# Optimization experiments

Hardware: AMD Instinct MI355X
Metric: run time of the kernel (lower is better)

## Reference

```python
import jax, jax.numpy as jnp
import numpy as np

N_NODES = 50000
N_EDGES = 1600000
N_FEAT = 4
N_GRAPHS = 128
K = 5


def setup_inputs() -> dict:
    key = jax.random.key(0)
    ks = jax.random.split(key, 16)
    x = jax.random.normal(ks[0], (N_NODES, N_FEAT), dtype=jnp.float32)
    edge_index = jax.random.randint(ks[1], (2, N_EDGES), 0, N_NODES, dtype=jnp.int64)
    batch = jnp.sort(jax.random.randint(ks[2], (N_NODES,), 0, N_GRAPHS, dtype=jnp.int64))
    def lin(k, shape):
        fan_in = shape[-2]
        return jax.random.normal(k, shape, dtype=jnp.float32) / np.sqrt(fan_in)
    return {
        "x": x,
        "edge_index": edge_index,
        "batch": batch,
        "num_graphs": N_GRAPHS,
        "W1": lin(ks[3], (K, N_FEAT, 32)), "b1": jnp.zeros((32,), jnp.float32),
        "W2": lin(ks[4], (K, 32, 64)),     "b2": jnp.zeros((64,), jnp.float32),
        "W3": lin(ks[5], (K, 64, 64)),     "b3": jnp.zeros((64,), jnp.float32),
        "fcw1": lin(ks[6], (64, 32)), "fcb1": jnp.zeros((32,), jnp.float32),
        "fcw2": lin(ks[7], (32, 1)),  "fcb2": jnp.zeros((1,), jnp.float32),
    }


def _cheb_conv(h, src, dst, w, Wk, b, n_nodes):
    # PyG ChebConv with sym norm, lambda_max=2:
    #   L_hat h = scatter_add(w_e * h[src_e] -> dst_e), w_e = -dinv[src]*dinv[dst]
    def L(z):
        return jax.ops.segment_sum(w[:, None] * z[src], dst, num_segments=n_nodes)
    Tx0 = h
    Tx1 = L(h)
    out = jnp.einsum('nf,fo->no', Tx0, Wk[0]) + jnp.einsum('nf,fo->no', Tx1, Wk[1])
    for k in range(2, Wk.shape[0]):
        Tx2 = 2.0 * L(Tx1) - Tx0
        out = out + jnp.einsum('nf,fo->no', Tx2, Wk[k])
        Tx0, Tx1 = Tx1, Tx2
    return out + b


def reference(x, edge_index, batch, num_graphs, W1, b1, W2, b2, W3, b3,
              fcw1, fcb1, fcw2, fcb2):
    n = x.shape[0]
    src, dst = edge_index[0], edge_index[1]
    # remove self loops (PyG ChebConv does remove_self_loops first)
    ew = (src != dst).astype(x.dtype)
    deg = jax.ops.segment_sum(ew, src, num_segments=n)
    dinv = jnp.where(deg > 0, jax.lax.rsqrt(jnp.where(deg > 0, deg, 1.0)), 0.0)
    w = -ew * dinv[src] * dinv[dst]  # scaled Laplacian off-diagonal; diagonal is 0

    h = jax.nn.relu(_cheb_conv(x, src, dst, w, W1, b1, n))
    h = jax.nn.relu(_cheb_conv(h, src, dst, w, W2, b2, n))
    h = jax.nn.relu(_cheb_conv(h, src, dst, w, W3, b3, n))

    # global_mean_pool over graph segments
    sums = jax.ops.segment_sum(h, batch, num_segments=num_graphs)
    cnts = jax.ops.segment_sum(jnp.ones((n,), h.dtype), batch, num_segments=num_graphs)
    pooled = sums / jnp.maximum(cnts, 1.0)[:, None]

    h = jax.nn.relu(pooled @ fcw1 + fcb1)
    return h @ fcw2 + fcb2
```

## Files before the change

kernel.cpp:

```cpp
#include <hip/hip_runtime.h>


constexpr int N_NODES  = 50000;
constexpr int N_EDGES  = 1600000;
constexpr int N_GRAPHS = 128;

constexpr int N16  = N_NODES * 16;
constexpr int SB32 = (N_NODES + 31) / 32;

constexpr int NB_H = 256;
constexpr int EPB  = N_EDGES / NB_H;
constexpr int NW   = (N_NODES + 3) / 4;

static inline int cdiv(long long a, int b) { return (int)((a + b - 1) / b); }


__global__ __launch_bounds__(256) void hist2_kernel(const int* __restrict__ src,
                                                    const int* __restrict__ dst,
                                                    unsigned* __restrict__ Hs,
                                                    unsigned* __restrict__ Hd) {
    extern __shared__ unsigned lds2[];
    unsigned* ls = lds2;
    unsigned* ld_ = lds2 + NW;
    const int b = blockIdx.x, t = threadIdx.x;
    for (int i = t; i < 2 * NW; i += 256) lds2[i] = 0;
    __syncthreads();
    const int e0 = b * EPB, e1 = e0 + EPB;
    for (int e = e0 + t; e < e1; e += 256) {
        int s = src[e], d = dst[e];
        if (s != d) {
            atomicAdd(&ls[s >> 2], 1u << (8 * (s & 3)));
            atomicAdd(&ld_[d >> 2], 1u << (8 * (d & 3)));
        }
    }
    __syncthreads();
    unsigned* HsB = Hs + (size_t)b * NW;
    unsigned* HdB = Hd + (size_t)b * NW;
    for (int i = t; i < NW; i += 256) { HsB[i] = ls[i]; HdB[i] = ld_[i]; }
}

__global__ void merge_src_kernel(const unsigned* __restrict__ H, float* __restrict__ dinv) {
    int i = blockIdx.x * blockDim.x + threadIdx.x;
    if (i >= NW) return;
    unsigned s0 = 0, s1 = 0, s2 = 0, s3 = 0;
    for (int b = 0; b < NB_H; ++b) {
        unsigned v = H[(size_t)b * NW + i];
        s0 += v & 0xff; s1 += (v >> 8) & 0xff; s2 += (v >> 16) & 0xff; s3 += v >> 24;
    }
    dinv[4 * i + 0] = s0 ? rsqrtf((float)s0) : 0.f;
    dinv[4 * i + 1] = s1 ? rsqrtf((float)s1) : 0.f;
    dinv[4 * i + 2] = s2 ? rsqrtf((float)s2) : 0.f;
    dinv[4 * i + 3] = s3 ? rsqrtf((float)s3) : 0.f;
}

__global__ void merge_dst_kernel(const unsigned* __restrict__ H, unsigned* __restrict__ P,
                                 int* __restrict__ cnt) {
    int i = blockIdx.x * blockDim.x + threadIdx.x;
    if (i >= NW) return;
    unsigned p0 = 0, p1 = 0, p2 = 0, p3 = 0;
    for (int b = 0; b < NB_H; ++b) {
        size_t idx = (size_t)b * NW + i;
        unsigned v = H[idx];
        P[idx] = p0 | (p1 << 8) | (p2 << 16) | (p3 << 24);
        p0 += v & 0xff; p1 += (v >> 8) & 0xff; p2 += (v >> 16) & 0xff; p3 += v >> 24;
    }
    cnt[4 * i + 0] = (int)p0; cnt[4 * i + 1] = (int)p1;
    cnt[4 * i + 2] = (int)p2; cnt[4 * i + 3] = (int)p3;
}


constexpr int SCAN_B = 256;
constexpr int SCAN_NB = (N_NODES + SCAN_B - 1) / SCAN_B;

__global__ void scan_block_kernel(const int* __restrict__ cnt, int* __restrict__ row,
                                  int* __restrict__ bsum) {
    __shared__ int buf[SCAN_B];
    int t = threadIdx.x;
    int i = blockIdx.x * SCAN_B + t;
    buf[t] = (i < N_NODES) ? cnt[i] : 0;
    __syncthreads();
    for (int off = 1; off < SCAN_B; off <<= 1) {
        int a = (t >= off) ? buf[t - off] : 0;
        __syncthreads();
        buf[t] += a;
        __syncthreads();
    }
    if (i < N_NODES) row[i + 1] = buf[t];
    if (t == SCAN_B - 1) bsum[blockIdx.x] = buf[t];
    if (i == 0) row[0] = 0;
}

__global__ void scan_sums_kernel(int* __restrict__ bsum) {
    __shared__ int buf[SCAN_NB];
    int t = threadIdx.x;
    if (t < SCAN_NB) buf[t] = bsum[t];
    __syncthreads();
    for (int off = 1; off < SCAN_NB; off <<= 1) {
        int a = (t >= off && t < SCAN_NB) ? buf[t - off] : 0;
        __syncthreads();
        if (t < SCAN_NB) buf[t] += a;
        __syncthreads();
    }
    if (t < SCAN_NB) bsum[t] = buf[t];
}

__global__ void scan_add_kernel(int* __restrict__ row, const int* __restrict__ bsum) {
    int i = blockIdx.x * SCAN_B + threadIdx.x;
    if (blockIdx.x > 0 && i < N_NODES) row[i + 1] += bsum[blockIdx.x - 1];
}

__global__ __launch_bounds__(256) void place_kernel(const int* __restrict__ src,
                                                    const int* __restrict__ dst,
                                                    const float* __restrict__ dinv,
                                                    const int* __restrict__ row,
                                                    const unsigned* __restrict__ P,
                                                    float2* __restrict__ csr) {
    __shared__ unsigned lds[NW];
    const int b = blockIdx.x, t = threadIdx.x;
    for (int i = t; i < NW; i += 256) lds[i] = 0;
    __syncthreads();
    const int e0 = b * EPB, e1 = e0 + EPB;
    const unsigned* Pb = P + (size_t)b * NW;
    for (int e = e0 + t; e < e1; e += 256) {
        int s = src[e], d = dst[e];
        if (s != d) {
            float w = -dinv[s] * dinv[d];
            int sh = 8 * (d & 3);
            unsigned old = atomicAdd(&lds[d >> 2], 1u << sh);
            unsigned cur = (old >> sh) & 0xff;
            unsigned pref = (Pb[d >> 2] >> sh) & 0xff;
            int pos = row[d] + (int)pref + (int)cur;
            csr[pos] = make_float2(w, __int_as_float(s));
        }
    }
}


__global__ void gatherF4_kernel(const int* __restrict__ row, const float2* __restrict__ csr,
                                const float* __restrict__ z, const float* __restrict__ prev,
                                float* __restrict__ out, float alpha, float beta) {
    int idx = blockIdx.x * blockDim.x + threadIdx.x;
    int node = idx >> 2;
    int lane = idx & 3;
    if (node >= N_NODES) return;
    int e0 = row[node], e1 = row[node + 1];
    float acc = 0.f;
#pragma unroll 4
    for (int e = e0; e < e1; ++e) {
        float2 ew = csr[e];
        acc = fmaf(ew.x, z[(size_t)__float_as_int(ew.y) * 4 + lane], acc);
    }
    float r = alpha * acc;
    if (beta != 0.f) r = fmaf(beta, prev[(size_t)node * 4 + lane], r);
    out[(size_t)node * 4 + lane] = r;
}

template <int NSLICE>
__global__ __launch_bounds__(128) void gather16_kernel(
        const int* __restrict__ row, const float2* __restrict__ csr,
        const float* __restrict__ z, const float* __restrict__ prev,
        float* __restrict__ out, float alpha, float beta) {
    constexpr int XPS = 8 / NSLICE;
    constexpr int CAP = 1024;
    __shared__ unsigned long long elds[CAP];
    const int bid = blockIdx.x;
    const int xcd = bid & 7;
    const int slice = xcd / XPS;
    const int sblk = (bid >> 3) * XPS + (xcd % XPS);
    if (sblk >= SB32) return;
    const int t = threadIdx.x;
    const int n = sblk * 32 + (t >> 2);
    const int lane = t & 3;
    const bool valid = (n < N_NODES);
    const float* zs = z + (size_t)slice * N16 + 4 * lane;
    const int e0 = valid ? row[n] : 0;
    const int e1 = valid ? row[n + 1] : 0;
    const int nb0 = sblk * 32;
    const int b0 = row[nb0];
    const int b1 = row[min(nb0 + 32, N_NODES)];
    float4 acc = make_float4(0.f, 0.f, 0.f, 0.f);
    for (int w0 = b0; w0 < b1; w0 += CAP) {
        const int w1 = min(w0 + CAP, b1);
        __syncthreads();
        for (int e = w0 + t; e < w1; e += 128)
            elds[e - w0] = __builtin_nontemporal_load((const unsigned long long*)csr + e);
        __syncthreads();
        const int g0 = max(e0, w0), g1 = min(e1, w1);
#pragma unroll 8
        for (int e = g0; e < g1; ++e) {
            unsigned long long raw = elds[e - w0];
            float w = __uint_as_float((unsigned)raw);
            int s = (int)(raw >> 32);
            const float4 zz = *(const float4*)(zs + (size_t)s * 16);
            acc.x = fmaf(w, zz.x, acc.x);
            acc.y = fmaf(w, zz.y, acc.y);
            acc.z = fmaf(w, zz.z, acc.z);
            acc.w = fmaf(w, zz.w, acc.w);
        }
    }
    if (valid) {
        float4 r = make_float4(alpha * acc.x, alpha * acc.y,
                               alpha * acc.z, alpha * acc.w);
        size_t off = (size_t)slice * N16 + (size_t)n * 16 + 4 * lane;
        if (beta != 0.f) {
            r.x = fmaf(beta, __builtin_nontemporal_load(prev + off), r.x);
            r.y = fmaf(beta, __builtin_nontemporal_load(prev + off + 1), r.y);
            r.z = fmaf(beta, __builtin_nontemporal_load(prev + off + 2), r.z);
            r.w = fmaf(beta, __builtin_nontemporal_load(prev + off + 3), r.w);
        }
        __builtin_nontemporal_store(r.x, out + off);
        __builtin_nontemporal_store(r.y, out + off + 1);
        __builtin_nontemporal_store(r.z, out + off + 2);
        __builtin_nontemporal_store(r.w, out + off + 3);
    }
}


template <int FI>
__global__ __launch_bounds__(256, 4) void combine64_kernel(
        const float* __restrict__ X, const float* __restrict__ T1,
        const float* __restrict__ T2, const float* __restrict__ T3,
        const float* __restrict__ T4, const float* __restrict__ W,
        const float* __restrict__ b, float* __restrict__ out) {
    constexpr int FO = 64;
    constexpr int TS = FI + 4;
    __shared__ float Ts[64 * TS];
    __shared__ float Ws[FI * FO];
    const int t = threadIdx.x;
    const int tn = t & 15;
    const int to = t >> 4;
    const int n_base = blockIdx.x * 64;
    const float* Tk[5] = {X, T1, T2, T3, T4};

    float acc[4][4];
    {
        const float4 bb = *(const float4*)(b + 4 * to);
#pragma unroll
        for (int i = 0; i < 4; ++i) {
            acc[i][0] = bb.x; acc[i][1] = bb.y; acc[i][2] = bb.z; acc[i][3] = bb.w;
        }
    }

#pragma unroll
    for (int k = 0; k < 5; ++k) {
        __syncthreads();
        {
            const float* base = Tk[k];
            constexpr int NV = 64 * FI / 4;
#pragma unroll
            for (int idx = t; idx < NV; idx += 256) {
                int r = idx / (FI / 4), c = idx % (FI / 4);
                int s = c >> 2;
                int j = (c & 3) * 4;
                float4 v = make_float4(0.f, 0.f, 0.f, 0.f);
                if (n_base + r < N_NODES)
                    v = *(const float4*)(base + (size_t)s * N16 +
                                         (size_t)(n_base + r) * 16 + j);
                *(float4*)(Ts + r * TS + 4 * c) = v;
            }
            const float4* w4 = (const float4*)(W + (size_t)k * FI * FO);
            constexpr int WV = FI * FO / 4;
#pragma unroll
            for (int idx = t; idx < WV; idx += 256) *(float4*)(Ws + 4 * idx) = w4[idx];
        }
        __syncthreads();
#pragma unroll 4
        for (int f0 = 0; f0 < FI; f0 += 4) {
            float tv[4][4];
#pragma unroll
            for (int i = 0; i < 4; ++i) {
                float4 q = *(const float4*)(Ts + (tn + 16 * i) * TS + f0);
                tv[i][0] = q.x; tv[i][1] = q.y; tv[i][2] = q.z; tv[i][3] = q.w;
            }
#pragma unroll
            for (int j = 0; j < 4; ++j) {
                float4 w = *(const float4*)(Ws + (f0 + j) * FO + 4 * to);
#pragma unroll
                for (int i = 0; i < 4; ++i) {
                    acc[i][0] = fmaf(tv[i][j], w.x, acc[i][0]);
                    acc[i][1] = fmaf(tv[i][j], w.y, acc[i][1]);
                    acc[i][2] = fmaf(tv[i][j], w.z, acc[i][2]);
                    acc[i][3] = fmaf(tv[i][j], w.w, acc[i][3]);
                }
            }
        }
    }
    __syncthreads();
#pragma unroll
    for (int i = 0; i < 4; ++i) {
        int n = n_base + tn + 16 * i;
        if (n < N_NODES) {
            float4 r = make_float4(fmaxf(acc[i][0], 0.f), fmaxf(acc[i][1], 0.f),
                                   fmaxf(acc[i][2], 0.f), fmaxf(acc[i][3], 0.f));
            int s = to >> 2;
            int j = (to & 3) * 4;
            *(float4*)(out + (size_t)s * N16 + (size_t)n * 16 + j) = r;
        }
    }
}

__global__ void combine432_kernel(const float* __restrict__ X, const float* __restrict__ T1,
                                  const float* __restrict__ T2, const float* __restrict__ T3,
                                  const float* __restrict__ T4, const float* __restrict__ W,
                                  const float* __restrict__ b, float* __restrict__ out) {
    __shared__ float Ws[5 * 4 * 32];
    int t = threadIdx.x;
    for (int i = t; i < 5 * 4 * 32; i += 256) Ws[i] = W[i];
    __syncthreads();
    int node = blockIdx.x * 8 + (t >> 5);
    int o = t & 31;
    if (node >= N_NODES) return;
    const float4* Tk[5] = {(const float4*)X, (const float4*)T1, (const float4*)T2,
                           (const float4*)T3, (const float4*)T4};
    float acc = b[o];
#pragma unroll
    for (int k = 0; k < 5; ++k) {
        float4 q = Tk[k][node];
        const float* w = Ws + k * 128 + o;
        acc = fmaf(q.x, w[0], acc);
        acc = fmaf(q.y, w[32], acc);
        acc = fmaf(q.z, w[64], acc);
        acc = fmaf(q.w, w[96], acc);
    }
    out[(size_t)(o >> 4) * N16 + (size_t)node * 16 + (o & 15)] = fmaxf(acc, 0.f);
}


__global__ void pool_kernel(const float* __restrict__ h, const int* __restrict__ batch,
                            float* __restrict__ pooled, float* __restrict__ cntf) {
    int wid = blockIdx.x * (blockDim.x / 64) + (threadIdx.x >> 6);
    int lane = threadIdx.x & 63;
    int nwaves = gridDim.x * (blockDim.x / 64);
    int per = (N_NODES + nwaves - 1) / nwaves;
    int n0 = wid * per;
    int n1 = min(n0 + per, N_NODES);
    if (n0 >= n1) return;
    const float* hp = h + (size_t)(lane >> 4) * N16 + (lane & 15);
    int cur = batch[n0];
    float acc = 0.f;
    int c = 0;
    for (int n = n0; n < n1; ++n) {
        int g = batch[n];
        if (g != cur) {
            atomicAdd(&pooled[cur * 64 + lane], acc);
            if (lane == 0) atomicAdd(&cntf[cur], (float)c);
            acc = 0.f; c = 0; cur = g;
        }
        acc += hp[(size_t)n * 16];
        ++c;
    }
    atomicAdd(&pooled[cur * 64 + lane], acc);
    if (lane == 0) atomicAdd(&cntf[cur], (float)c);
}

__global__ void fc_kernel(const float* __restrict__ pooled, const float* __restrict__ cnt,
                          const float* __restrict__ w1, const float* __restrict__ b1,
                          const float* __restrict__ w2, const float* __restrict__ b2,
                          float* __restrict__ out) {
    int g = blockIdx.x;
    int t = threadIdx.x;
    __shared__ float hid[32];
    float c = fmaxf(cnt[g], 1.0f);
    float acc = b1[t];
    for (int f = 0; f < 64; ++f) acc = fmaf(pooled[g * 64 + f] / c, w1[f * 32 + t], acc);
    hid[t] = fmaxf(acc, 0.f);
    __syncthreads();
    if (t == 0) {
        float acc2 = b2[0];
        for (int o = 0; o < 32; ++o) acc2 = fmaf(hid[o], w2[o], acc2);
        out[g] = acc2;
    }
}


template <int FI, int FO>
static void run_layer(const int* row, const float2* csr, const float* X,
                      float* T1, float* T2, float* T3, float* T4,
                      const float* W, const float* b, float* out, hipStream_t stream) {
    if constexpr (FI == 4) {
        dim3 g(cdiv((long long)N_NODES * 4, 256)), blk(256);
        hipLaunchKernelGGL(gatherF4_kernel, g, blk, 0, stream, row, csr, X,  X,  T1, 1.f, 0.f);
        hipLaunchKernelGGL(gatherF4_kernel, g, blk, 0, stream, row, csr, T1, X,  T2, 2.f, -1.f);
        hipLaunchKernelGGL(gatherF4_kernel, g, blk, 0, stream, row, csr, T2, T1, T3, 2.f, -1.f);
        hipLaunchKernelGGL(gatherF4_kernel, g, blk, 0, stream, row, csr, T3, T2, T4, 2.f, -1.f);
    } else {
        constexpr int NSLICE = FI / 16;
        constexpr int XPS = 8 / NSLICE;
        dim3 g(cdiv(SB32, XPS) * 8), blk(128);
        hipLaunchKernelGGL((gather16_kernel<NSLICE>), g, blk, 0, stream, row, csr, X,  X,  T1, 1.f, 0.f);
        hipLaunchKernelGGL((gather16_kernel<NSLICE>), g, blk, 0, stream, row, csr, T1, X,  T2, 2.f, -1.f);
        hipLaunchKernelGGL((gather16_kernel<NSLICE>), g, blk, 0, stream, row, csr, T2, T1, T3, 2.f, -1.f);
        hipLaunchKernelGGL((gather16_kernel<NSLICE>), g, blk, 0, stream, row, csr, T3, T2, T4, 2.f, -1.f);
    }
    if constexpr (FO == 64) {
        hipLaunchKernelGGL((combine64_kernel<FI>), dim3(cdiv(N_NODES, 64)), dim3(256), 0,
                           stream, X, T1, T2, T3, T4, W, b, out);
    } else {
        hipLaunchKernelGGL(combine432_kernel, dim3(cdiv(N_NODES, 8)), dim3(256), 0,
                           stream, X, T1, T2, T3, T4, W, b, out);
    }
}

extern "C" void kernel_launch(void* const* d_in, const int* in_sizes, int n_in,
                              void* d_out, int out_size, void* d_ws, size_t ws_size,
                              hipStream_t stream) {
    const float* x    = (const float*)d_in[0];
    const int*   ei   = (const int*)d_in[1];
    const int*   batch= (const int*)d_in[2];
    const float* W1   = (const float*)d_in[4];
    const float* b1   = (const float*)d_in[5];
    const float* W2   = (const float*)d_in[6];
    const float* b2   = (const float*)d_in[7];
    const float* W3   = (const float*)d_in[8];
    const float* b3   = (const float*)d_in[9];
    const float* fcw1 = (const float*)d_in[10];
    const float* fcb1 = (const float*)d_in[11];
    const float* fcw2 = (const float*)d_in[12];
    const float* fcb2 = (const float*)d_in[13];

    const int* src = ei;
    const int* dst = ei + N_EDGES;

    float* base = (float*)d_ws;
    float*  dinv   = base + 0;
    int*    cnt_i  = (int*)(base + 50000);
    int*    row    = (int*)(base + 100000);
    int*    bsum   = (int*)(base + 150004);
    float2* csr    = (float2*)(base + 150256);
    float*  T1     = base + 3350256;
    float*  T2     = base + 6550256;
    float*  T3     = base + 9750256;
    float*  T4     = base + 12950256;
    float*  H1     = T4 + 1600000;
    float*  H2     = base + 16150256;
    float*  pooled = base + 19350256;
    float*  cntf   = base + 19358448;

    unsigned* Hs = (unsigned*)T1;
    unsigned* Hd = (unsigned*)T2;
    unsigned* P  = (unsigned*)T3;

    hipLaunchKernelGGL(hist2_kernel, dim3(NB_H), dim3(256), 2 * NW * sizeof(unsigned),
                       stream, src, dst, Hs, Hd);
    hipLaunchKernelGGL(merge_src_kernel, dim3(cdiv(NW, 256)), dim3(256), 0, stream, Hs, dinv);
    hipLaunchKernelGGL(merge_dst_kernel, dim3(cdiv(NW, 256)), dim3(256), 0, stream, Hd, P, cnt_i);
    hipLaunchKernelGGL(scan_block_kernel, dim3(SCAN_NB), dim3(SCAN_B), 0, stream, cnt_i, row, bsum);
    hipLaunchKernelGGL(scan_sums_kernel, dim3(1), dim3(256), 0, stream, bsum);
    hipLaunchKernelGGL(scan_add_kernel, dim3(SCAN_NB), dim3(SCAN_B), 0, stream, row, bsum);
    hipLaunchKernelGGL(place_kernel, dim3(NB_H), dim3(256), 0, stream,
                       src, dst, dinv, row, P, csr);

    run_layer<4, 32>(row, csr, x,  T1, T2, T3, T4, W1, b1, H1, stream);
    run_layer<32, 64>(row, csr, H1, T1, T2, T3, T4, W2, b2, H2, stream);
    run_layer<64, 64>(row, csr, H2, T1, T2, T3, T4, W3, b3, T1, stream);

    hipMemsetAsync(pooled, 0, (8192 + 128) * sizeof(float), stream);
    hipLaunchKernelGGL(pool_kernel, dim3(128), dim3(256), 0, stream, T1, batch, pooled, cntf);
    hipLaunchKernelGGL(fc_kernel, dim3(N_GRAPHS), dim3(32), 0, stream,
                       pooled, cntf, fcw1, fcb1, fcw2, fcb2, (float*)d_out);
}
```

Before: 695.4 us.

## Switch feature storage from 16-wide to 32-wide node slices for gathers

Changes the sliced feature layout from 16-float slices to 32-float slices across the gather, combine and pooling kernels. Each gather block now covers 32 nodes with 8 lanes each and 256 threads, and the CSR edge window per block is doubled. Layer 2 now runs in a single slice pass and layer 3 in two XCD-mapped slices, so the CSR edge list is streamed half as many times. The trade-off is a larger per-node gather footprint (128 bytes per source row), which may lower cache locality.

```diff
diff --git a/kernel.cpp b/kernel.cpp
--- a/kernel.cpp
+++ b/kernel.cpp
@@ -5,7 +5,7 @@
 constexpr int N_EDGES  = 1600000;
 constexpr int N_GRAPHS = 128;
 
-constexpr int N16  = N_NODES * 16;
+constexpr int NF   = N_NODES * 32;
 constexpr int SB32 = (N_NODES + 31) / 32;
 
 constexpr int NB_H = 256;
@@ -156,23 +156,27 @@
 }
 
 template <int NSLICE>
-__global__ __launch_bounds__(128) void gather16_kernel(
+__global__ __launch_bounds__(256) void gather32_kernel(
         const int* __restrict__ row, const float2* __restrict__ csr,
         const float* __restrict__ z, const float* __restrict__ prev,
         float* __restrict__ out, float alpha, float beta) {
-    constexpr int XPS = 8 / NSLICE;
-    constexpr int CAP = 1024;
+    constexpr int CAP = 2048;
     __shared__ unsigned long long elds[CAP];
-    const int bid = blockIdx.x;
-    const int xcd = bid & 7;
-    const int slice = xcd / XPS;
-    const int sblk = (bid >> 3) * XPS + (xcd % XPS);
+    int sblk, slice;
+    if constexpr (NSLICE == 1) {
+        sblk = blockIdx.x;
+        slice = 0;
+    } else {
+        const int xcd = blockIdx.x & 7;
+        slice = xcd >> 2;
+        sblk = (blockIdx.x >> 3) * 4 + (xcd & 3);
+    }
     if (sblk >= SB32) return;
     const int t = threadIdx.x;
-    const int n = sblk * 32 + (t >> 2);
-    const int lane = t & 3;
+    const int n = sblk * 32 + (t >> 3);
+    const int lane = t & 7;
     const bool valid = (n < N_NODES);
-    const float* zs = z + (size_t)slice * N16 + 4 * lane;
+    const float* zs = z + (size_t)slice * NF + 4 * lane;
     const int e0 = valid ? row[n] : 0;
     const int e1 = valid ? row[n + 1] : 0;
     const int nb0 = sblk * 32;
@@ -182,7 +186,7 @@
     for (int w0 = b0; w0 < b1; w0 += CAP) {
         const int w1 = min(w0 + CAP, b1);
         __syncthreads();
-        for (int e = w0 + t; e < w1; e += 128)
+        for (int e = w0 + t; e < w1; e += 256)
             elds[e - w0] = __builtin_nontemporal_load((const unsigned long long*)csr + e);
         __syncthreads();
         const int g0 = max(e0, w0), g1 = min(e1, w1);
@@ -191,7 +195,7 @@
             unsigned long long raw = elds[e - w0];
             float w = __uint_as_float((unsigned)raw);
             int s = (int)(raw >> 32);
-            const float4 zz = *(const float4*)(zs + (size_t)s * 16);
+            const float4 zz = *(const float4*)(zs + (size_t)s * 32);
             acc.x = fmaf(w, zz.x, acc.x);
             acc.y = fmaf(w, zz.y, acc.y);
             acc.z = fmaf(w, zz.z, acc.z);
@@ -201,7 +205,7 @@
     if (valid) {
         float4 r = make_float4(alpha * acc.x, alpha * acc.y,
                                alpha * acc.z, alpha * acc.w);
-        size_t off = (size_t)slice * N16 + (size_t)n * 16 + 4 * lane;
+        size_t off = (size_t)slice * NF + (size_t)n * 32 + 4 * lane;
         if (beta != 0.f) {
             r.x = fmaf(beta, __builtin_nontemporal_load(prev + off), r.x);
             r.y = fmaf(beta, __builtin_nontemporal_load(prev + off + 1), r.y);
@@ -250,12 +254,12 @@
 #pragma unroll
             for (int idx = t; idx < NV; idx += 256) {
                 int r = idx / (FI / 4), c = idx % (FI / 4);
-                int s = c >> 2;
-                int j = (c & 3) * 4;
+                int s = c >> 3;
+                int j = (c & 7) * 4;
                 float4 v = make_float4(0.f, 0.f, 0.f, 0.f);
                 if (n_base + r < N_NODES)
-                    v = *(const float4*)(base + (size_t)s * N16 +
-                                         (size_t)(n_base + r) * 16 + j);
+                    v = *(const float4*)(base + (size_t)s * NF +
+                                         (size_t)(n_base + r) * 32 + j);
                 *(float4*)(Ts + r * TS + 4 * c) = v;
             }
             const float4* w4 = (const float4*)(W + (size_t)k * FI * FO);
@@ -292,9 +296,9 @@
         if (n < N_NODES) {
             float4 r = make_float4(fmaxf(acc[i][0], 0.f), fmaxf(acc[i][1], 0.f),
                                    fmaxf(acc[i][2], 0.f), fmaxf(acc[i][3], 0.f));
-            int s = to >> 2;
-            int j = (to & 3) * 4;
-            *(float4*)(out + (size_t)s * N16 + (size_t)n * 16 + j) = r;
+            int s = to >> 3;
+            int j = (to & 7) * 4;
+            *(float4*)(out + (size_t)s * NF + (size_t)n * 32 + j) = r;
         }
     }
 }
@@ -322,7 +326,7 @@
         acc = fmaf(q.z, w[64], acc);
         acc = fmaf(q.w, w[96], acc);
     }
-    out[(size_t)(o >> 4) * N16 + (size_t)node * 16 + (o & 15)] = fmaxf(acc, 0.f);
+    out[(size_t)node * 32 + o] = fmaxf(acc, 0.f);
 }
 
 
@@ -335,7 +339,7 @@
     int n0 = wid * per;
     int n1 = min(n0 + per, N_NODES);
     if (n0 >= n1) return;
-    const float* hp = h + (size_t)(lane >> 4) * N16 + (lane & 15);
+    const float* hp = h + (size_t)(lane >> 5) * NF + (lane & 31);
     int cur = batch[n0];
     float acc = 0.f;
     int c = 0;
@@ -346,7 +350,7 @@
             if (lane == 0) atomicAdd(&cntf[cur], (float)c);
             acc = 0.f; c = 0; cur = g;
         }
-        acc += hp[(size_t)n * 16];
+        acc += hp[(size_t)n * 32];
         ++c;
     }
     atomicAdd(&pooled[cur * 64 + lane], acc);
@@ -384,13 +388,12 @@
         hipLaunchKernelGGL(gatherF4_kernel, g, blk, 0, stream, row, csr, T2, T1, T3, 2.f, -1.f);
         hipLaunchKernelGGL(gatherF4_kernel, g, blk, 0, stream, row, csr, T3, T2, T4, 2.f, -1.f);
     } else {
-        constexpr int NSLICE = FI / 16;
-        constexpr int XPS = 8 / NSLICE;
-        dim3 g(cdiv(SB32, XPS) * 8), blk(128);
-        hipLaunchKernelGGL((gather16_kernel<NSLICE>), g, blk, 0, stream, row, csr, X,  X,  T1, 1.f, 0.f);
-        hipLaunchKernelGGL((gather16_kernel<NSLICE>), g, blk, 0, stream, row, csr, T1, X,  T2, 2.f, -1.f);
-        hipLaunchKernelGGL((gather16_kernel<NSLICE>), g, blk, 0, stream, row, csr, T2, T1, T3, 2.f, -1.f);
-        hipLaunchKernelGGL((gather16_kernel<NSLICE>), g, blk, 0, stream, row, csr, T3, T2, T4, 2.f, -1.f);
+        constexpr int NSLICE = FI / 32;
+        dim3 g(NSLICE == 1 ? SB32 : cdiv(SB32, 4) * 8), blk(256);
+        hipLaunchKernelGGL((gather32_kernel<NSLICE>), g, blk, 0, stream, row, csr, X,  X,  T1, 1.f, 0.f);
+        hipLaunchKernelGGL((gather32_kernel<NSLICE>), g, blk, 0, stream, row, csr, T1, X,  T2, 2.f, -1.f);
+        hipLaunchKernelGGL((gather32_kernel<NSLICE>), g, blk, 0, stream, row, csr, T2, T1, T3, 2.f, -1.f);
+        hipLaunchKernelGGL((gather32_kernel<NSLICE>), g, blk, 0, stream, row, csr, T3, T2, T4, 2.f, -1.f);
     }
     if constexpr (FO == 64) {
         hipLaunchKernelGGL((combine64_kernel<FI>), dim3(cdiv(N_NODES, 64)), dim3(256), 0,
```

Result: slower. 715.3 us (+2.9%).
